# Kernel optimization log

Measured on AMD Instinct MI355X. Metric: run time of the kernel, lower is better.

The kernel has to match this reference:

```python
import jax, jax.numpy as jnp
import numpy as np

D_MODEL = 1024
N_HEADS = 16
D_HEAD = D_MODEL // N_HEADS
WIN = 256
NEG_INF = -1e30


def setup_inputs() -> dict:
    key = jax.random.key(0)
    k1, k2, k3 = jax.random.split(key, 3)
    B, L = 4, 4096
    x = jax.random.normal(k1, (B, L, D_MODEL), dtype=jnp.float32)
    w_qkv = jax.random.normal(k2, (D_MODEL, 3 * D_MODEL), dtype=jnp.float32) * (1.0 / np.sqrt(D_MODEL))
    w_out = jax.random.normal(k3, (D_MODEL, D_MODEL), dtype=jnp.float32) * (1.0 / np.sqrt(D_MODEL))
    return {"x": x, "w_qkv": w_qkv, "w_out": w_out}


def _band_mask(nb: int):
    ti = jnp.arange(WIN)[:, None]
    tj = jnp.arange(2 * WIN)[None, :]
    base = (tj >= ti + 1) & (tj <= ti + WIN)
    first = base & (tj >= WIN)                         # block 0 has zero-padded (invalid) prev block
    rest = jnp.broadcast_to(base, (nb - 1, WIN, 2 * WIN))
    return jnp.concatenate([first[None], rest], axis=0)


def reference(x, w_qkv, w_out):
    B, L, D = x.shape
    nb = L // WIN
    qkv = (x @ w_qkv).reshape(B, L, 3, N_HEADS, D_HEAD)
    q, k, v = qkv[:, :, 0], qkv[:, :, 1], qkv[:, :, 2]          # [B, L, H, dh]
    def to_blocks(t):
        return t.transpose(0, 2, 1, 3).reshape(B, N_HEADS, nb, WIN, D_HEAD)
    qb, kb, vb = to_blocks(q), to_blocks(k), to_blocks(v)
    zero_blk = jnp.zeros_like(kb[:, :, :1])
    k_kv = jnp.concatenate([jnp.concatenate([zero_blk, kb[:, :, :-1]], axis=2), kb], axis=3)  # [B,H,nb,2W,dh]
    v_kv = jnp.concatenate([jnp.concatenate([zero_blk, vb[:, :, :-1]], axis=2), vb], axis=3)
    scale = 1.0 / np.sqrt(D_HEAD)
    scores = jnp.einsum('bhnqd,bhnkd->bhnqk', qb, k_kv) * scale
    scores = jnp.where(_band_mask(nb), scores, NEG_INF)
    attn = jax.nn.softmax(scores, axis=-1)
    ob = jnp.einsum('bhnqk,bhnkd->bhnqd', attn, v_kv)
    out = ob.reshape(B, N_HEADS, L, D_HEAD).transpose(0, 2, 1, 3).reshape(B, L, D)
    return out @ w_out
```

## Files before the change

kernel.cpp:

```cpp
#include <hip/hip_runtime.h>

typedef __bf16 bf16_t;
typedef __bf16 bf16x8 __attribute__((ext_vector_type(8)));
typedef float f32x4 __attribute__((ext_vector_type(4)));
typedef unsigned short ushort_t;

#define MFMA_16x16x32(a, b, c) __builtin_amdgcn_mfma_f32_16x16x32_bf16((a), (b), (c), 0, 0, 0)

__device__ __forceinline__ void async_ld16(const void* gptr, void* lptr) {
  typedef __attribute__((address_space(1))) const unsigned int as1_t;
  typedef __attribute__((address_space(3))) unsigned int as3_t;
  __builtin_amdgcn_global_load_lds((as1_t*)(unsigned long long)gptr,
                                   (as3_t*)(unsigned int)(unsigned long long)lptr,
                                   16, 0, 0);
}

__global__ void detect_dtype(const ushort_t* __restrict__ x, int* __restrict__ flag) {
  __shared__ int cnt[256];
  int c = 0;
#pragma unroll
  for (int i = 0; i < 16; ++i) {
    const ushort_t u = x[threadIdx.x * 16 + i];
    const int e = (u >> 7) & 0xFF;
    if ((u & 0x7FFF) != 0 && (e < 0x3A || e > 0xC0)) ++c;
  }
  cnt[threadIdx.x] = c;
  __syncthreads();
  if (threadIdx.x == 0) {
    int t = 0;
    for (int i = 0; i < 256; ++i) t += cnt[i];
    *flag = (t > 512) ? 1 : 0;
  }
}

__global__ __launch_bounds__(256) void convert_to_bf16(const void* __restrict__ src,
                                                       bf16_t* __restrict__ dst, int n8,
                                                       const int* __restrict__ flag) {
  const int isF32 = *flag;
  int i = blockIdx.x * 256 + threadIdx.x;
  const int stride = gridDim.x * 256;
  if (isF32) {
    const float4* s = (const float4*)src;
    for (; i < n8; i += stride) {
      const float4 a = s[(size_t)i * 2];
      const float4 b = s[(size_t)i * 2 + 1];
      bf16x8 o;
      o[0] = (bf16_t)a.x; o[1] = (bf16_t)a.y; o[2] = (bf16_t)a.z; o[3] = (bf16_t)a.w;
      o[4] = (bf16_t)b.x; o[5] = (bf16_t)b.y; o[6] = (bf16_t)b.z; o[7] = (bf16_t)b.w;
      *(bf16x8*)(dst + (size_t)i * 8) = o;
    }
  } else {
    const uint4* s = (const uint4*)src;
    for (; i < n8; i += stride) ((uint4*)dst)[i] = s[i];
  }
}

__global__ __launch_bounds__(256) void transpose_b16(const ushort_t* __restrict__ in,
                                                     ushort_t* __restrict__ out,
                                                     int R, int C) {
  __shared__ alignas(16) ushort_t t[64 * 72];
  const int tid = threadIdx.x;
  const int c0 = blockIdx.x * 64;
  const int r0 = blockIdx.y * 64;
#pragma unroll
  for (int it = 0; it < 2; ++it) {
    int cid = tid + it * 256;
    int row = cid >> 3, co = (cid & 7) * 8;
    *(uint4*)(t + row * 72 + co) = *(const uint4*)(in + (size_t)(r0 + row) * C + c0 + co);
  }
  __syncthreads();
#pragma unroll
  for (int it = 0; it < 2; ++it) {
    int cid = tid + it * 256;
    int orow = cid >> 3, ko = (cid & 7) * 8;
    uint4 u;
    ushort_t* tp = (ushort_t*)&u;
#pragma unroll
    for (int j = 0; j < 8; ++j) tp[j] = t[(ko + j) * 72 + orow];
    *(uint4*)(out + (size_t)(c0 + orow) * R + r0 + ko) = u;
  }
}

__global__ __launch_bounds__(256) void transpose_v(const ushort_t* __restrict__ qkv,
                                                   ushort_t* __restrict__ vT) {
  __shared__ alignas(16) ushort_t t[64 * 72];
  const int tid = threadIdx.x;
  const int l0 = blockIdx.x * 64;
  const int bh = blockIdx.y;
  const int b = bh >> 4, h = bh & 15;
  const ushort_t* src = qkv + ((size_t)(b * 4096 + l0)) * 3072 + 2048 + h * 64;
#pragma unroll
  for (int it = 0; it < 2; ++it) {
    int cid = tid + it * 256;
    int row = cid >> 3, co = (cid & 7) * 8;
    *(uint4*)(t + row * 72 + co) = *(const uint4*)(src + (size_t)row * 3072 + co);
  }
  __syncthreads();
  ushort_t* dst = vT + ((size_t)bh * 64) * 4096 + l0;
#pragma unroll
  for (int it = 0; it < 2; ++it) {
    int cid = tid + it * 256;
    int d = cid >> 3, ko = (cid & 7) * 8;
    uint4 u;
    ushort_t* tp = (ushort_t*)&u;
#pragma unroll
    for (int j = 0; j < 8; ++j) tp[j] = t[(ko + j) * 72 + d];
    *(uint4*)(dst + (size_t)d * 4096 + ko) = u;
  }
}

__global__ __launch_bounds__(256) void gemm_bf16(const bf16_t* __restrict__ A, int lda,
                                                 const bf16_t* __restrict__ Bt,
                                                 void* __restrict__ Cout, int N_out,
                                                 int K, const int* __restrict__ flag) {
  __shared__ alignas(16) bf16_t smem[8192];
  bf16_t* a_lds = smem;
  bf16_t* b_lds = smem + 4096;
  const int tid = threadIdx.x;
  const int wave = tid >> 6;
  const int lane = tid & 63;
  const int l15 = lane & 15;
  const int quad = lane >> 4;
  const int tm = blockIdx.y * 128;
  const int tn = blockIdx.x * 128;
  const int wm = (wave >> 1) * 64;
  const int wn = (wave & 1) * 64;

  f32x4 acc[4][4];
#pragma unroll
  for (int i = 0; i < 4; ++i)
#pragma unroll
    for (int j = 0; j < 4; ++j) acc[i][j] = (f32x4){0.f, 0.f, 0.f, 0.f};

  const int srow = wave * 32 + (lane >> 2);
  const int scol = (lane & 3) * 8;
  const bf16_t* ag = A + (size_t)(tm + srow) * lda + scol;
  const bf16_t* bg = Bt + (size_t)(tn + srow) * K + scol;
  bf16_t* al = a_lds + (wave * 32) * 32;
  bf16_t* bl = b_lds + (wave * 32) * 32;

  for (int k0 = 0; k0 < K; k0 += 32) {
    __syncthreads();
    async_ld16(ag, al);
    async_ld16(ag + (size_t)16 * lda, al + 16 * 32);
    async_ld16(bg, bl);
    async_ld16(bg + (size_t)16 * K, bl + 16 * 32);
    ag += 32;
    bg += 32;
    __syncthreads();

    bf16x8 af[4], bfr[4];
#pragma unroll
    for (int i = 0; i < 4; ++i)
      af[i] = *(const bf16x8*)(a_lds + (wm + i * 16 + l15) * 32 + quad * 8);
#pragma unroll
    for (int j = 0; j < 4; ++j)
      bfr[j] = *(const bf16x8*)(b_lds + (wn + j * 16 + l15) * 32 + quad * 8);
#pragma unroll
    for (int i = 0; i < 4; ++i)
#pragma unroll
      for (int j = 0; j < 4; ++j) acc[i][j] = MFMA_16x16x32(af[i], bfr[j], acc[i][j]);
  }
  __syncthreads();

  const int isF32 = flag ? *flag : 0;
  if (isF32) {
#pragma unroll
    for (int i = 0; i < 4; ++i) {
      const int m = tm + wm + i * 16 + quad * 4;
#pragma unroll
      for (int j = 0; j < 4; ++j) {
        const int n = tn + wn + j * 16 + l15;
        float* cp = (float*)Cout + (size_t)m * N_out + n;
#pragma unroll
        for (int r = 0; r < 4; ++r) cp[(size_t)r * N_out] = acc[i][j][r];
      }
    }
  } else {
    bf16_t* stg = smem + wave * 1152;
#pragma unroll
    for (int i = 0; i < 4; ++i) {
#pragma unroll
      for (int j = 0; j < 4; ++j)
#pragma unroll
        for (int r = 0; r < 4; ++r)
          stg[(quad * 4 + r) * 72 + j * 16 + l15] = (bf16_t)acc[i][j][r];
      __asm__ volatile("s_waitcnt lgkmcnt(0)" ::: "memory");
      const int m0 = tm + wm + i * 16;
#pragma unroll
      for (int p = 0; p < 2; ++p) {
        const int idx = lane + p * 64;
        const int row = idx >> 3, c8 = (idx & 7) * 8;
        uint4 u = *(const uint4*)(stg + row * 72 + c8);
        *(uint4*)((bf16_t*)Cout + (size_t)(m0 + row) * N_out + tn + wn + c8) = u;
      }
      __asm__ volatile("s_waitcnt lgkmcnt(0)" ::: "memory");
    }
  }
}

__global__ __launch_bounds__(256) void attn_swa(bf16_t* qkv, const bf16_t* __restrict__ vT) {
  __shared__ alignas(16) bf16_t k_lds[64 * 72];
  __shared__ alignas(16) bf16_t vt_lds[64 * 72];
  __shared__ alignas(16) bf16_t p_lds[4 * 16 * 72];

  const int wg = blockIdx.x;
  const int b = wg >> 10;
  const int h = (wg >> 6) & 15;
  const int qt = wg & 63;
  const int blk = qt >> 2;
  const int wq = qt & 3;
  const int tid = threadIdx.x;
  const int wave = tid >> 6;
  const int lane = tid & 63;
  const int l15 = lane & 15;
  const int quad = lane >> 4;
  const int qw = qt * 64 + wave * 16;

  const size_t qoff = ((size_t)(b * 4096 + qw + l15)) * 3072 + h * 64;
  const bf16x8 qf0 = *(const bf16x8*)(qkv + qoff + quad * 8);
  const bf16x8 qf1 = *(const bf16x8*)(qkv + qoff + 32 + quad * 8);

  f32x4 of[4];
#pragma unroll
  for (int i = 0; i < 4; ++i) of[i] = (f32x4){0.f, 0.f, 0.f, 0.f};
  float m_i[4], l_i[4];
#pragma unroll
  for (int r = 0; r < 4; ++r) {
    m_i[r] = -1e30f;
    l_i[r] = 0.0f;
  }

  const int kb0 = blk * 256 - 256;
  const int kclo = (blk == 0) ? 4 : wq;
  const int kchi = wq + 4;

  for (int kc = kclo; kc <= kchi; ++kc) {
    const int kb = kb0 + kc * 64;
    __syncthreads();
#pragma unroll
    for (int it = 0; it < 2; ++it) {
      int cid = tid + it * 256;
      int row = cid >> 3;
      int co = (cid & 7) * 8;
      *(uint4*)(k_lds + row * 72 + co) =
          *(const uint4*)(qkv + ((size_t)(b * 4096 + kb + row)) * 3072 + 1024 + h * 64 + co);
      *(uint4*)(vt_lds + row * 72 + co) =
          *(const uint4*)(vT + (((size_t)b * 16 + h) * 64 + row) * 4096 + kb + co);
    }
    __syncthreads();

    f32x4 s[4];
#pragma unroll
    for (int nt = 0; nt < 4; ++nt) {
      bf16x8 kf0 = *(const bf16x8*)(k_lds + (nt * 16 + l15) * 72 + quad * 8);
      bf16x8 kf1 = *(const bf16x8*)(k_lds + (nt * 16 + l15) * 72 + 32 + quad * 8);
      f32x4 z = (f32x4){0.f, 0.f, 0.f, 0.f};
      z = MFMA_16x16x32(qf0, kf0, z);
      z = MFMA_16x16x32(qf1, kf1, z);
      s[nt] = z;
    }

    float sv[4][4];
#pragma unroll
    for (int nt = 0; nt < 4; ++nt) {
      const int key = kb + nt * 16 + l15;
#pragma unroll
      for (int r = 0; r < 4; ++r) {
        const int p = qw + quad * 4 + r;
        const bool valid = (key <= p) && (key + 256 > p);
        sv[nt][r] = valid ? s[nt][r] * 0.125f : -1e30f;
      }
    }
    float rm[4];
#pragma unroll
    for (int r = 0; r < 4; ++r)
      rm[r] = fmaxf(fmaxf(sv[0][r], sv[1][r]), fmaxf(sv[2][r], sv[3][r]));
#pragma unroll
    for (int off = 1; off < 16; off <<= 1)
#pragma unroll
      for (int r = 0; r < 4; ++r) rm[r] = fmaxf(rm[r], __shfl_xor(rm[r], off));

    float mn[4], alpha[4];
#pragma unroll
    for (int r = 0; r < 4; ++r) {
      mn[r] = fmaxf(m_i[r], rm[r]);
      alpha[r] = __expf(m_i[r] - mn[r]);
      m_i[r] = mn[r];
    }

    float rs[4] = {0.f, 0.f, 0.f, 0.f};
#pragma unroll
    for (int nt = 0; nt < 4; ++nt)
#pragma unroll
      for (int r = 0; r < 4; ++r) {
        const float pv = (sv[nt][r] > -1e29f) ? __expf(sv[nt][r] - mn[r]) : 0.0f;
        rs[r] += pv;
        p_lds[wave * 1152 + (quad * 4 + r) * 72 + nt * 16 + l15] = (bf16_t)pv;
      }
#pragma unroll
    for (int off = 1; off < 16; off <<= 1)
#pragma unroll
      for (int r = 0; r < 4; ++r) rs[r] += __shfl_xor(rs[r], off);
#pragma unroll
    for (int r = 0; r < 4; ++r) l_i[r] = l_i[r] * alpha[r] + rs[r];
#pragma unroll
    for (int dt = 0; dt < 4; ++dt)
#pragma unroll
      for (int r = 0; r < 4; ++r) of[dt][r] *= alpha[r];

    __syncthreads();

#pragma unroll
    for (int kk = 0; kk < 2; ++kk) {
      bf16x8 pf = *(const bf16x8*)(p_lds + wave * 1152 + l15 * 72 + kk * 32 + quad * 8);
#pragma unroll
      for (int dt = 0; dt < 4; ++dt) {
        bf16x8 vf = *(const bf16x8*)(vt_lds + (dt * 16 + l15) * 72 + kk * 32 + quad * 8);
        of[dt] = MFMA_16x16x32(pf, vf, of[dt]);
      }
    }
  }

  float inv[4];
#pragma unroll
  for (int r = 0; r < 4; ++r) inv[r] = 1.0f / fmaxf(l_i[r], 1e-20f);
  bf16_t* op = qkv + ((size_t)(b * 4096 + qw)) * 3072 + h * 64;
#pragma unroll
  for (int dt = 0; dt < 4; ++dt)
#pragma unroll
    for (int r = 0; r < 4; ++r)
      op[(size_t)(quad * 4 + r) * 3072 + dt * 16 + l15] = (bf16_t)(of[dt][r] * inv[r]);
}

extern "C" void kernel_launch(void* const* d_in, const int* in_sizes, int n_in,
                              void* d_out, int out_size, void* d_ws, size_t ws_size,
                              hipStream_t stream) {
  char* ws = (char*)d_ws;
  bf16_t* wTq = (bf16_t*)(ws);
  bf16_t* wTo = (bf16_t*)(ws + 6291456);
  bf16_t* qkv = (bf16_t*)(ws + 8388608);
  int* flag = (int*)(ws + 109051904);

  bf16_t* xb = (bf16_t*)d_out;
  bf16_t* vTb = (bf16_t*)d_out;
  bf16_t* tmpq = qkv;
  bf16_t* tmpo = qkv + 3145728;

  detect_dtype<<<1, 256, 0, stream>>>((const ushort_t*)d_in[0], flag);
  convert_to_bf16<<<1024, 256, 0, stream>>>(d_in[0], xb, 2097152, flag);
  convert_to_bf16<<<512, 256, 0, stream>>>(d_in[1], tmpq, 393216, flag);
  convert_to_bf16<<<256, 256, 0, stream>>>(d_in[2], tmpo, 131072, flag);
  transpose_b16<<<dim3(48, 16), 256, 0, stream>>>((const ushort_t*)tmpq, (ushort_t*)wTq,
                                                  1024, 3072);
  transpose_b16<<<dim3(16, 16), 256, 0, stream>>>((const ushort_t*)tmpo, (ushort_t*)wTo,
                                                  1024, 1024);
  gemm_bf16<<<dim3(24, 128), 256, 0, stream>>>(xb, 1024, wTq, qkv, 3072, 1024, nullptr);
  transpose_v<<<dim3(64, 64), 256, 0, stream>>>((const ushort_t*)qkv, (ushort_t*)vTb);
  attn_swa<<<dim3(4096), 256, 0, stream>>>(qkv, vTb);
  gemm_bf16<<<dim3(8, 128), 256, 0, stream>>>(qkv, 3072, wTo, d_out, 1024, 1024, flag);
}
```

Measured before the change: 432.6 us.

## Swizzle GEMM LDS layout, templatize dims, skip masks on interior attention tiles

The GEMM now takes its leading dimensions as template parameters so address math is compile-time constant. Its global-to-LDS load columns and the fragment reads are XOR-swizzled to cut LDS bank conflicts. In attention, tiles lying entirely inside the window skip the per-element mask and validity checks. The scale is folded with log2(e) so exp2f replaces __expf. Together these target LDS conflict stalls and ALU overhead in the softmax, at the cost of more code paths and a swizzle that must match between writer and reader.

```diff
diff --git a/kernel.cpp b/kernel.cpp
--- a/kernel.cpp
+++ b/kernel.cpp
@@ -109,10 +109,11 @@
   }
 }
 
-__global__ __launch_bounds__(256) void gemm_bf16(const bf16_t* __restrict__ A, int lda,
+template <int LDA, int KK, int NOUT>
+__global__ __launch_bounds__(256) void gemm_bf16(const bf16_t* __restrict__ A,
                                                  const bf16_t* __restrict__ Bt,
-                                                 void* __restrict__ Cout, int N_out,
-                                                 int K, const int* __restrict__ flag) {
+                                                 void* __restrict__ Cout,
+                                                 const int* __restrict__ flag) {
   __shared__ alignas(16) bf16_t smem[8192];
   bf16_t* a_lds = smem;
   bf16_t* b_lds = smem + 4096;
@@ -133,18 +134,20 @@
     for (int j = 0; j < 4; ++j) acc[i][j] = (f32x4){0.f, 0.f, 0.f, 0.f};
 
   const int srow = wave * 32 + (lane >> 2);
-  const int scol = (lane & 3) * 8;
-  const bf16_t* ag = A + (size_t)(tm + srow) * lda + scol;
-  const bf16_t* bg = Bt + (size_t)(tn + srow) * K + scol;
+  const int scol = (((lane & 3) ^ ((lane >> 3) & 3))) * 8;
+  const bf16_t* ag = A + (size_t)(tm + srow) * LDA + scol;
+  const bf16_t* bg = Bt + (size_t)(tn + srow) * KK + scol;
   bf16_t* al = a_lds + (wave * 32) * 32;
   bf16_t* bl = b_lds + (wave * 32) * 32;
 
-  for (int k0 = 0; k0 < K; k0 += 32) {
+  const int sw8 = (quad ^ ((l15 >> 1) & 3)) * 8;
+
+  for (int k0 = 0; k0 < KK; k0 += 32) {
     __syncthreads();
     async_ld16(ag, al);
-    async_ld16(ag + (size_t)16 * lda, al + 16 * 32);
+    async_ld16(ag + (size_t)16 * LDA, al + 16 * 32);
     async_ld16(bg, bl);
-    async_ld16(bg + (size_t)16 * K, bl + 16 * 32);
+    async_ld16(bg + (size_t)16 * KK, bl + 16 * 32);
     ag += 32;
     bg += 32;
     __syncthreads();
@@ -152,10 +155,10 @@
     bf16x8 af[4], bfr[4];
 #pragma unroll
     for (int i = 0; i < 4; ++i)
-      af[i] = *(const bf16x8*)(a_lds + (wm + i * 16 + l15) * 32 + quad * 8);
+      af[i] = *(const bf16x8*)(a_lds + (wm + i * 16 + l15) * 32 + sw8);
 #pragma unroll
     for (int j = 0; j < 4; ++j)
-      bfr[j] = *(const bf16x8*)(b_lds + (wn + j * 16 + l15) * 32 + quad * 8);
+      bfr[j] = *(const bf16x8*)(b_lds + (wn + j * 16 + l15) * 32 + sw8);
 #pragma unroll
     for (int i = 0; i < 4; ++i)
 #pragma unroll
@@ -171,9 +174,9 @@
 #pragma unroll
       for (int j = 0; j < 4; ++j) {
         const int n = tn + wn + j * 16 + l15;
-        float* cp = (float*)Cout + (size_t)m * N_out + n;
-#pragma unroll
-        for (int r = 0; r < 4; ++r) cp[(size_t)r * N_out] = acc[i][j][r];
+        float* cp = (float*)Cout + (size_t)m * NOUT + n;
+#pragma unroll
+        for (int r = 0; r < 4; ++r) cp[(size_t)r * NOUT] = acc[i][j][r];
       }
     }
   } else {
@@ -192,7 +195,7 @@
         const int idx = lane + p * 64;
         const int row = idx >> 3, c8 = (idx & 7) * 8;
         uint4 u = *(const uint4*)(stg + row * 72 + c8);
-        *(uint4*)((bf16_t*)Cout + (size_t)(m0 + row) * N_out + tn + wn + c8) = u;
+        *(uint4*)((bf16_t*)Cout + (size_t)(m0 + row) * NOUT + tn + wn + c8) = u;
       }
       __asm__ volatile("s_waitcnt lgkmcnt(0)" ::: "memory");
     }
@@ -203,6 +206,8 @@
   __shared__ alignas(16) bf16_t k_lds[64 * 72];
   __shared__ alignas(16) bf16_t vt_lds[64 * 72];
   __shared__ alignas(16) bf16_t p_lds[4 * 16 * 72];
+
+  const float SC = 0.125f * 1.44269504089f;
 
   const int wg = blockIdx.x;
   const int b = wg >> 10;
@@ -261,17 +266,27 @@
       s[nt] = z;
     }
 
+    const bool interior = (kc <= wq + 3) && (blk == 0 || kc >= wq + 1);
+
     float sv[4][4];
-#pragma unroll
-    for (int nt = 0; nt < 4; ++nt) {
-      const int key = kb + nt * 16 + l15;
-#pragma unroll
-      for (int r = 0; r < 4; ++r) {
-        const int p = qw + quad * 4 + r;
-        const bool valid = (key <= p) && (key + 256 > p);
-        sv[nt][r] = valid ? s[nt][r] * 0.125f : -1e30f;
+    if (interior) {
+#pragma unroll
+      for (int nt = 0; nt < 4; ++nt)
+#pragma unroll
+        for (int r = 0; r < 4; ++r) sv[nt][r] = s[nt][r] * SC;
+    } else {
+#pragma unroll
+      for (int nt = 0; nt < 4; ++nt) {
+        const int key = kb + nt * 16 + l15;
+#pragma unroll
+        for (int r = 0; r < 4; ++r) {
+          const int p = qw + quad * 4 + r;
+          const bool valid = (key <= p) && (key + 256 > p);
+          sv[nt][r] = valid ? s[nt][r] * SC : -1e30f;
+        }
       }
     }
+
     float rm[4];
 #pragma unroll
     for (int r = 0; r < 4; ++r)
@@ -285,19 +300,30 @@
 #pragma unroll
     for (int r = 0; r < 4; ++r) {
       mn[r] = fmaxf(m_i[r], rm[r]);
-      alpha[r] = __expf(m_i[r] - mn[r]);
+      alpha[r] = exp2f(m_i[r] - mn[r]);
       m_i[r] = mn[r];
     }
 
     float rs[4] = {0.f, 0.f, 0.f, 0.f};
-#pragma unroll
-    for (int nt = 0; nt < 4; ++nt)
-#pragma unroll
-      for (int r = 0; r < 4; ++r) {
-        const float pv = (sv[nt][r] > -1e29f) ? __expf(sv[nt][r] - mn[r]) : 0.0f;
-        rs[r] += pv;
-        p_lds[wave * 1152 + (quad * 4 + r) * 72 + nt * 16 + l15] = (bf16_t)pv;
-      }
+    if (interior) {
+#pragma unroll
+      for (int nt = 0; nt < 4; ++nt)
+#pragma unroll
+        for (int r = 0; r < 4; ++r) {
+          const float pv = exp2f(sv[nt][r] - mn[r]);
+          rs[r] += pv;
+          p_lds[wave * 1152 + (quad * 4 + r) * 72 + nt * 16 + l15] = (bf16_t)pv;
+        }
+    } else {
+#pragma unroll
+      for (int nt = 0; nt < 4; ++nt)
+#pragma unroll
+        for (int r = 0; r < 4; ++r) {
+          const float pv = (sv[nt][r] > -1e29f) ? exp2f(sv[nt][r] - mn[r]) : 0.0f;
+          rs[r] += pv;
+          p_lds[wave * 1152 + (quad * 4 + r) * 72 + nt * 16 + l15] = (bf16_t)pv;
+        }
+    }
 #pragma unroll
     for (int off = 1; off < 16; off <<= 1)
 #pragma unroll
@@ -355,8 +381,8 @@
                                                   1024, 3072);
   transpose_b16<<<dim3(16, 16), 256, 0, stream>>>((const ushort_t*)tmpo, (ushort_t*)wTo,
                                                   1024, 1024);
-  gemm_bf16<<<dim3(24, 128), 256, 0, stream>>>(xb, 1024, wTq, qkv, 3072, 1024, nullptr);
+  gemm_bf16<1024, 1024, 3072><<<dim3(24, 128), 256, 0, stream>>>(xb, wTq, qkv, nullptr);
   transpose_v<<<dim3(64, 64), 256, 0, stream>>>((const ushort_t*)qkv, (ushort_t*)vTb);
   attn_swa<<<dim3(4096), 256, 0, stream>>>(qkv, vTb);
-  gemm_bf16<<<dim3(8, 128), 256, 0, stream>>>(qkv, 3072, wTo, d_out, 1024, 1024, flag);
-}
+  gemm_bf16<3072, 1024, 1024><<<dim3(8, 128), 256, 0, stream>>>(qkv, wTo, d_out, flag);
+}
```

Result: slower. 447.5 us (+3.4%).
